# Optimization experiments

Measured on AMD Instinct MI355X. Metric: run time of the kernel, lower is better.

## Reference

```python
import jax, jax.numpy as jnp
import numpy as np

N_NODES = 100000
N_EDGES = 3200000
D_NODE = 16
D_EDGE = 8
D_HIDDEN = 16


def setup_inputs() -> dict:
    key = jax.random.key(0)
    ks = jax.random.split(key, 8)
    node_features = jax.random.normal(ks[0], (N_NODES, D_NODE), dtype=jnp.float32)
    edge_attr_e3nn = jax.random.normal(ks[1], (N_EDGES, D_EDGE), dtype=jnp.float32)
    node_attr_scalar_raw = jax.random.normal(ks[2], (N_NODES, 1), dtype=jnp.float32)
    W_msg_tp = jax.random.normal(ks[3], (D_NODE, D_EDGE, D_HIDDEN), dtype=jnp.float32)
    W_msg_lin = jax.random.normal(ks[4], (D_HIDDEN, D_HIDDEN), dtype=jnp.float32)
    W_upd_tp = jax.random.normal(ks[5], (D_NODE, D_HIDDEN, D_HIDDEN), dtype=jnp.float32)
    W_upd_lin = jax.random.normal(ks[6], (D_HIDDEN, D_NODE), dtype=jnp.float32)
    edge_index = jax.random.randint(ks[7], (2, N_EDGES), 0, N_NODES, dtype=jnp.int64)
    return {
        "node_features": node_features,
        "edge_attr_e3nn": edge_attr_e3nn,
        "node_attr_scalar_raw": node_attr_scalar_raw,
        "W_msg_tp": W_msg_tp,
        "W_msg_lin": W_msg_lin,
        "W_upd_tp": W_upd_tp,
        "W_upd_lin": W_upd_lin,
        "edge_index": edge_index,
    }


def reference(node_features, edge_attr_e3nn, node_attr_scalar_raw,
              W_msg_tp, W_msg_lin, W_upd_tp, W_upd_lin, edge_index):
    n_nodes = node_features.shape[0]
    row = edge_index[0]  # destination (aggregation target)
    col = edge_index[1]  # source (gathered neighbor)

    # fan-in normalizations (e3nn FullyConnectedTensorProduct / Linear convention)
    norm_msg_tp = 1.0 / np.float32(np.sqrt(D_NODE * D_EDGE))
    norm_upd_tp = 1.0 / np.float32(np.sqrt(D_NODE * D_HIDDEN))
    norm_lin = 1.0 / np.float32(np.sqrt(D_HIDDEN))

    # --- message step: gather -> bilinear TP -> gate -> linear ---
    x_j = node_features[col]                                   # [E, D_node]
    m = jnp.einsum('ei,ej,ijh->eh', x_j, edge_attr_e3nn, W_msg_tp) * norm_msg_tp
    m = jax.nn.silu(m)                                         # gate nonlinearity
    m = (m @ W_msg_lin) * norm_lin                             # [E, D_hidden]

    # --- scatter-sum aggregation into nodes ---
    agg = jax.ops.segment_sum(m, row, num_segments=n_nodes)    # [N, D_hidden]

    # --- update step: bilinear TP -> gate -> linear -> residual ---
    u = jnp.einsum('ni,nh,ihk->nk', node_features, agg, W_upd_tp) * norm_upd_tp
    u = jax.nn.silu(u)
    u = (u @ W_upd_lin) * norm_lin                             # [N, D_node]

    return node_features + u
```

## Files before the change

### kernel.cpp

```cpp
#include <hip/hip_runtime.h>
#include <math.h>

#define N_NODES_C 100000
#define N_EDGES_C 3200000

#define NORM_MSG_TP 0.08838834764831845f
#define NORM_UPD_TP 0.0625f
#define NORM_LIN    0.25f

typedef float f32x4 __attribute__((ext_vector_type(4)));
typedef short bf16x8 __attribute__((ext_vector_type(8)));

__device__ __forceinline__ float silu_f(float v) {
  return v / (1.0f + __expf(-v));
}

__device__ __forceinline__ void atomic_add_hw(float* p, float v) {
  unsafeAtomicAdd(p, v);
}

__device__ __forceinline__ unsigned int bf16_bits(float f) {
  unsigned int b = __float_as_uint(f);
  return (b + 0x7fffu + ((b >> 16) & 1u)) >> 16;
}
__device__ __forceinline__ unsigned int pack_bf16x2(float lo, float hi) {
  return bf16_bits(lo) | (bf16_bits(hi) << 16);
}
__device__ __forceinline__ float unlo(unsigned int w) { return __uint_as_float(w << 16); }
__device__ __forceinline__ float unhi(unsigned int w) { return __uint_as_float(w & 0xffff0000u); }


__global__ __launch_bounds__(256) void zero_ints(int* __restrict__ p, int n) {
  int i = blockIdx.x * 256 + threadIdx.x;
  if (i < n) p[i] = 0;
}

__global__ __launch_bounds__(256) void hist_kernel(
    const int* __restrict__ row, int* __restrict__ cnt) {
  int e = blockIdx.x * 256 + threadIdx.x;
  atomicAdd(&cnt[row[e]], 1);
}

__global__ __launch_bounds__(256) void scan_block(
    const int* __restrict__ cnt, int* __restrict__ off, int* __restrict__ bsum, int n) {
  __shared__ int s[256];
  const int t = threadIdx.x;
  const int i = blockIdx.x * 256 + t;
  const int v = (i < n) ? cnt[i] : 0;
  s[t] = v;
  __syncthreads();
#pragma unroll
  for (int o = 1; o < 256; o <<= 1) {
    int tv = (t >= o) ? s[t - o] : 0;
    __syncthreads();
    s[t] += tv;
    __syncthreads();
  }
  if (i < n) off[i] = s[t] - v;
  if (t == 255) bsum[blockIdx.x] = s[255];
}

__global__ void scan_bsum(int* __restrict__ bsum, int nb) {
  __shared__ int s[512];
  const int t = threadIdx.x;
  const int v = (t < nb) ? bsum[t] : 0;
  s[t] = v;
  __syncthreads();
#pragma unroll
  for (int o = 1; o < 512; o <<= 1) {
    int tv = (t >= o) ? s[t - o] : 0;
    __syncthreads();
    s[t] += tv;
    __syncthreads();
  }
  if (t < nb) bsum[t] = s[t] - v;
}

__global__ __launch_bounds__(256) void scan_add(
    int* __restrict__ off, const int* __restrict__ bsum, int n, int total) {
  int i = blockIdx.x * 256 + threadIdx.x;
  if (i < n) off[i] += bsum[blockIdx.x];
  if (i == 0) off[n] = total;
}


__global__ __launch_bounds__(256) void xcast_kernel(
    const float* __restrict__ x, unsigned short* __restrict__ xb) {
  const int i = blockIdx.x * 256 + threadIdx.x;
  if (i < N_NODES_C * 2) {
    const float4 a = *reinterpret_cast<const float4*>(x + (size_t)i * 8);
    const float4 b = *reinterpret_cast<const float4*>(x + (size_t)i * 8 + 4);
    uint4 w;
    w.x = pack_bf16x2(a.x, a.y); w.y = pack_bf16x2(a.z, a.w);
    w.z = pack_bf16x2(b.x, b.y); w.w = pack_bf16x2(b.z, b.w);
    *reinterpret_cast<uint4*>(xb + (size_t)i * 8) = w;
  }
}


__global__ __launch_bounds__(256) void place3_kernel(
    const int*   __restrict__ eidx,
    const float* __restrict__ ea,
    const float* __restrict__ Wtp,
    const int*   __restrict__ off,
    int*         __restrict__ cnt,
    const unsigned short* __restrict__ xb,
    unsigned int* __restrict__ msort)
{
  __shared__ float sm[4][16][16];
  const int lane = threadIdx.x & 63;
  const int wv   = threadIdx.x >> 6;
  const int r    = lane & 15;
  const int g    = lane >> 4;

  bf16x8 bq[4];
#pragma unroll
  for (int q = 0; q < 4; ++q) {
#pragma unroll
    for (int t = 0; t < 8; ++t) {
      const float w = Wtp[(32 * q + g * 8 + t) * 16 + r];
      bq[q][t] = (short)bf16_bits(w);
    }
  }

  const int nwaves = gridDim.x * 4;
  const int wid = blockIdx.x * 4 + wv;
  const int ntiles = N_EDGES_C / 16;

  for (int tile = wid; tile < ntiles; tile += nwaves) {
    const int e = tile * 16 + r;

    int pp = 0;
    if (g == 0) {
      const int rd = eidx[e];
      pp = off[rd] + atomicSub(&cnt[rd], 1) - 1;
    }

    const int c = eidx[N_EDGES_C + e];
    const float4 ja = *reinterpret_cast<const float4*>(ea + (size_t)e * 8);
    const float4 jb = *reinterpret_cast<const float4*>(ea + (size_t)e * 8 + 4);

    f32x4 acc = {0.f, 0.f, 0.f, 0.f};
#pragma unroll
    for (int q = 0; q < 4; ++q) {
      const float xs = __uint_as_float(
          (unsigned int)xb[(size_t)c * 16 + 4 * q + g] << 16);
      bf16x8 af;
      af[0] = (short)bf16_bits(xs * ja.x);
      af[1] = (short)bf16_bits(xs * ja.y);
      af[2] = (short)bf16_bits(xs * ja.z);
      af[3] = (short)bf16_bits(xs * ja.w);
      af[4] = (short)bf16_bits(xs * jb.x);
      af[5] = (short)bf16_bits(xs * jb.y);
      af[6] = (short)bf16_bits(xs * jb.z);
      af[7] = (short)bf16_bits(xs * jb.w);
      acc = __builtin_amdgcn_mfma_f32_16x16x32_bf16(af, bq[q], acc, 0, 0, 0);
    }

#pragma unroll
    for (int j2 = 0; j2 < 4; ++j2)
      sm[wv][g * 4 + j2][r] = silu_f(acc[j2] * NORM_MSG_TP);

    asm volatile("s_waitcnt lgkmcnt(0)" ::: "memory");
    __builtin_amdgcn_sched_barrier(0);

    const int rr  = lane >> 2;
    const int wsl = lane & 3;
    const float4 v4 = *reinterpret_cast<const float4*>(&sm[wv][rr][wsl * 4]);
    const int p_rr = __shfl(pp, rr);
    uint2 wout;
    wout.x = pack_bf16x2(v4.x, v4.y);
    wout.y = pack_bf16x2(v4.z, v4.w);
    *reinterpret_cast<uint2*>(&msort[(size_t)p_rr * 8 + wsl * 2]) = wout;
  }
}


__global__ __launch_bounds__(256) void agg3_kernel(
    const float* __restrict__ Wlin,
    const unsigned int* __restrict__ msort,
    const int*   __restrict__ off,
    float*       __restrict__ agg)
{
  __shared__ float sL[256];
  if (threadIdx.x < 256) sL[threadIdx.x] = Wlin[threadIdx.x];
  __syncthreads();

  const int slane = threadIdx.x & 15;
  const int n = blockIdx.x * 16 + (threadIdx.x >> 4);

  const int off0 = off[n];
  const int off1 = off[n + 1];

  float acc = 0.f;
  for (int p = off0; p < off1; ++p) {
    const unsigned int w = msort[(size_t)p * 8 + (slane >> 1)];
    acc += (slane & 1) ? unhi(w) : unlo(w);
  }

  float a = 0.f;
#pragma unroll
  for (int h = 0; h < 16; ++h) {
    const float v = __shfl(acc, h, 16);
    a = fmaf(v, sL[h * 16 + slane], a);
  }
  agg[(size_t)n * 16 + slane] = a * NORM_LIN;
}


__global__ __launch_bounds__(256) void tbuild_kernel(
    const float* __restrict__ x, const float* __restrict__ Wtp,
    uint4* __restrict__ Tb)
{
  __shared__ float sWT[16 * 132];
  for (int idx = threadIdx.x; idx < 2048; idx += 256) {
    const int i = idx >> 7, j = (idx >> 4) & 7, h = idx & 15;
    sWT[h * 132 + i * 8 + j] = Wtp[idx];
  }
  __syncthreads();

  const int slane = threadIdx.x & 15;
  const int n = blockIdx.x * 16 + (threadIdx.x >> 4);

  float xr[16];
  const float4* xp = reinterpret_cast<const float4*>(x + (size_t)n * 16);
#pragma unroll
  for (int q = 0; q < 4; ++q) {
    float4 v = xp[q];
    xr[q*4+0] = v.x; xr[q*4+1] = v.y; xr[q*4+2] = v.z; xr[q*4+3] = v.w;
  }

  float t[8];
#pragma unroll
  for (int j = 0; j < 8; ++j) t[j] = 0.f;
#pragma unroll
  for (int i = 0; i < 16; ++i) {
    const float xi = xr[i];
    const float4 wa = *reinterpret_cast<const float4*>(&sWT[slane * 132 + i * 8]);
    const float4 wb = *reinterpret_cast<const float4*>(&sWT[slane * 132 + i * 8 + 4]);
    t[0] = fmaf(xi, wa.x, t[0]); t[1] = fmaf(xi, wa.y, t[1]);
    t[2] = fmaf(xi, wa.z, t[2]); t[3] = fmaf(xi, wa.w, t[3]);
    t[4] = fmaf(xi, wb.x, t[4]); t[5] = fmaf(xi, wb.y, t[5]);
    t[6] = fmaf(xi, wb.z, t[6]); t[7] = fmaf(xi, wb.w, t[7]);
  }
  uint4 w;
  w.x = pack_bf16x2(t[0], t[1]);
  w.y = pack_bf16x2(t[2], t[3]);
  w.z = pack_bf16x2(t[4], t[5]);
  w.w = pack_bf16x2(t[6], t[7]);
  Tb[(size_t)n * 16 + slane] = w;
}

__global__ __launch_bounds__(256) void place_kernel(
    const int* __restrict__ eidx, const float* __restrict__ ea,
    const int* __restrict__ off, int* __restrict__ cnt,
    int* __restrict__ colp, uint4* __restrict__ eab) {
  int e = blockIdx.x * 256 + threadIdx.x;
  const int r = eidx[e];
  const int old = atomicSub(&cnt[r], 1);
  const int p = off[r] + old - 1;
  colp[p] = eidx[N_EDGES_C + e];
  const float4* ep = reinterpret_cast<const float4*>(ea + (size_t)e * 8);
  const float4 a = ep[0];
  const float4 b = ep[1];
  uint4 w;
  w.x = pack_bf16x2(a.x, a.y);
  w.y = pack_bf16x2(a.z, a.w);
  w.z = pack_bf16x2(b.x, b.y);
  w.w = pack_bf16x2(b.z, b.w);
  eab[p] = w;
}

__global__ __launch_bounds__(256) void agg2_kernel(
    const float* __restrict__ Wlin, const int* __restrict__ colp,
    const uint4* __restrict__ eab, const uint4* __restrict__ Tb,
    const int* __restrict__ off, float* __restrict__ agg)
{
  __shared__ float sL[256];
  if (threadIdx.x < 256) sL[threadIdx.x] = Wlin[threadIdx.x];
  __syncthreads();

  const int slane = threadIdx.x & 15;
  const int n = blockIdx.x * 16 + (threadIdx.x >> 4);

  const int off0 = off[n];
  const int off1 = off[n + 1];

  float acc = 0.f;
#pragma unroll 2
  for (int p = off0; p < off1; ++p) {
    const int c = colp[p];
    const uint4 tw = Tb[(size_t)c * 16 + slane];
    const uint4 ew = eab[p];
    float m;
    m  = unlo(ew.x) * unlo(tw.x);
    m  = fmaf(unhi(ew.x), unhi(tw.x), m);
    m  = fmaf(unlo(ew.y), unlo(tw.y), m);
    m  = fmaf(unhi(ew.y), unhi(tw.y), m);
    m  = fmaf(unlo(ew.z), unlo(tw.z), m);
    m  = fmaf(unhi(ew.z), unhi(tw.z), m);
    m  = fmaf(unlo(ew.w), unlo(tw.w), m);
    m  = fmaf(unhi(ew.w), unhi(tw.w), m);
    acc += silu_f(m * NORM_MSG_TP);
  }

  float a = 0.f;
#pragma unroll
  for (int h = 0; h < 16; ++h) {
    const float v = __shfl(acc, h, 16);
    a = fmaf(v, sL[h * 16 + slane], a);
  }
  agg[(size_t)n * 16 + slane] = a * NORM_LIN;
}


__global__ __launch_bounds__(256) void node_kernel(
    const float* __restrict__ x, const float* __restrict__ agg,
    const float* __restrict__ Wtp, const float* __restrict__ Wlin,
    float* __restrict__ out)
{
  __shared__ float sW[4096];
  __shared__ float sL[256];
  for (int t = threadIdx.x; t < 4096; t += 256) sW[t] = Wtp[t];
  sL[threadIdx.x] = Wlin[threadIdx.x];
  __syncthreads();

  const long n = (long)blockIdx.x * 256 + threadIdx.x;
  if (n >= N_NODES_C) return;

  float xr[16], ar[16];
  const float4* xp = reinterpret_cast<const float4*>(x + (size_t)n * 16);
  const float4* ap = reinterpret_cast<const float4*>(agg + (size_t)n * 16);
#pragma unroll
  for (int q = 0; q < 4; ++q) {
    float4 v = xp[q];
    xr[q*4+0] = v.x; xr[q*4+1] = v.y; xr[q*4+2] = v.z; xr[q*4+3] = v.w;
    float4 w = ap[q];
    ar[q*4+0] = w.x; ar[q*4+1] = w.y; ar[q*4+2] = w.z; ar[q*4+3] = w.w;
  }
  float u[16];
#pragma unroll
  for (int k = 0; k < 16; ++k) u[k] = 0.f;
#pragma unroll
  for (int i = 0; i < 16; ++i) {
#pragma unroll
    for (int h = 0; h < 16; ++h) {
      const float p = xr[i] * ar[h];
      const float* w = &sW[(i*16 + h) * 16];
#pragma unroll
      for (int k = 0; k < 16; ++k) u[k] = fmaf(p, w[k], u[k]);
    }
  }
  float g[16];
#pragma unroll
  for (int k = 0; k < 16; ++k) g[k] = silu_f(u[k] * NORM_UPD_TP);
  float res[16];
#pragma unroll
  for (int k2 = 0; k2 < 16; ++k2) {
    float a = 0.f;
#pragma unroll
    for (int k = 0; k < 16; ++k) a = fmaf(g[k], sL[k*16 + k2], a);
    res[k2] = xr[k2] + a * NORM_LIN;
  }
  float4* op = reinterpret_cast<float4*>(out + (size_t)n * 16);
#pragma unroll
  for (int q = 0; q < 4; ++q)
    op[q] = make_float4(res[q*4+0], res[q*4+1], res[q*4+2], res[q*4+3]);
}


__global__ void zero_f4(float4* __restrict__ p, int n4) {
  int i = blockIdx.x * blockDim.x + threadIdx.x;
  if (i < n4) p[i] = make_float4(0.f, 0.f, 0.f, 0.f);
}

#define EPT 2
__global__ __launch_bounds__(256) void edge_kernel(
    const float* __restrict__ x, const float* __restrict__ ea,
    const float* __restrict__ Wtp, const float* __restrict__ Wlin,
    const int* __restrict__ eidx, float* __restrict__ agg)
{
  __shared__ float sW[2048];
  __shared__ float sL[256];
  for (int t = threadIdx.x; t < 2048; t += 256) sW[t] = Wtp[t];
  sL[threadIdx.x] = Wlin[threadIdx.x];
  __syncthreads();
  const long e0 = ((long)blockIdx.x * 256 + threadIdx.x) * EPT;
  float xr[EPT][16], er[EPT][8];
  int rw[EPT];
#pragma unroll
  for (int e = 0; e < EPT; ++e) {
    const long ei = e0 + e;
    const int c = eidx[N_EDGES_C + ei];
    rw[e] = eidx[ei];
    const float4* xp = reinterpret_cast<const float4*>(x + (size_t)c * 16);
#pragma unroll
    for (int q = 0; q < 4; ++q) {
      float4 v = xp[q];
      xr[e][q*4+0] = v.x; xr[e][q*4+1] = v.y; xr[e][q*4+2] = v.z; xr[e][q*4+3] = v.w;
    }
    const float4* ep = reinterpret_cast<const float4*>(ea + (size_t)ei * 8);
#pragma unroll
    for (int q = 0; q < 2; ++q) {
      float4 v = ep[q];
      er[e][q*4+0] = v.x; er[e][q*4+1] = v.y; er[e][q*4+2] = v.z; er[e][q*4+3] = v.w;
    }
  }
  float m[EPT][16];
#pragma unroll
  for (int e = 0; e < EPT; ++e)
#pragma unroll
    for (int h = 0; h < 16; ++h) m[e][h] = 0.f;
#pragma unroll
  for (int i = 0; i < 16; ++i) {
#pragma unroll
    for (int j = 0; j < 8; ++j) {
      float p[EPT];
#pragma unroll
      for (int e = 0; e < EPT; ++e) p[e] = xr[e][i] * er[e][j];
      const float* w = &sW[(i*8 + j) * 16];
#pragma unroll
      for (int h = 0; h < 16; ++h) {
        const float wv = w[h];
#pragma unroll
        for (int e = 0; e < EPT; ++e) m[e][h] = fmaf(p[e], wv, m[e][h]);
      }
    }
  }
#pragma unroll
  for (int e = 0; e < EPT; ++e) {
    float g[16];
#pragma unroll
    for (int h = 0; h < 16; ++h) g[h] = silu_f(m[e][h] * NORM_MSG_TP);
    float* ap = agg + (size_t)rw[e] * 16;
#pragma unroll
    for (int h2 = 0; h2 < 16; ++h2) {
      float a = 0.f;
#pragma unroll
      for (int h = 0; h < 16; ++h) a = fmaf(g[h], sL[h*16 + h2], a);
      atomic_add_hw(ap + h2, a * NORM_LIN);
    }
  }
}


extern "C" void kernel_launch(void* const* d_in, const int* in_sizes, int n_in,
                              void* d_out, int out_size, void* d_ws, size_t ws_size,
                              hipStream_t stream) {
  const float* node_features = (const float*)d_in[0];
  const float* edge_attr     = (const float*)d_in[1];
  const float* W_msg_tp      = (const float*)d_in[3];
  const float* W_msg_lin     = (const float*)d_in[4];
  const float* W_upd_tp      = (const float*)d_in[5];
  const float* W_upd_lin     = (const float*)d_in[6];
  const int*   edge_index    = (const int*)d_in[7];
  float* out = (float*)d_out;
  char* ws = (char*)d_ws;

  const int NB_N = (N_NODES_C + 255) / 256;
  const int NB_E = N_EDGES_C / 256;
  const int NB_G = N_NODES_C / 16;

  const size_t A_OFF  = 0;
  const size_t A_CNT  = 400128;
  const size_t A_BSUM = 800256;
  const size_t A_MSORT= 802304;
  const size_t A_XB   = A_MSORT + 102400000;
  const size_t A_AGG  = A_XB + 3200000;
  const size_t A_NEED = A_AGG + 6400000;

  const size_t B_OFF  = 0;
  const size_t B_CNT  = 400128;
  const size_t B_BSUM = 800256;
  const size_t B_COLP = 804352;
  const size_t B_EAB  = B_COLP + 12800000;
  const size_t B_T    = B_EAB + 51200000;
  const size_t B_AGG  = B_T + 25600000;
  const size_t B_NEED = B_AGG + 6400000;

  if (ws_size >= A_NEED) {
    int*   off   = (int*)(ws + A_OFF);
    int*   cnt   = (int*)(ws + A_CNT);
    int*   bsum  = (int*)(ws + A_BSUM);
    unsigned int* msort = (unsigned int*)(ws + A_MSORT);
    unsigned short* xb  = (unsigned short*)(ws + A_XB);
    float* agg   = (float*)(ws + A_AGG);

    hipLaunchKernelGGL(zero_ints, dim3(NB_N), dim3(256), 0, stream, cnt, N_NODES_C);
    hipLaunchKernelGGL(hist_kernel, dim3(NB_E), dim3(256), 0, stream, edge_index, cnt);
    hipLaunchKernelGGL(scan_block, dim3(NB_N), dim3(256), 0, stream,
                       cnt, off, bsum, N_NODES_C);
    hipLaunchKernelGGL(scan_bsum, dim3(1), dim3(512), 0, stream, bsum, NB_N);
    hipLaunchKernelGGL(scan_add, dim3(NB_N), dim3(256), 0, stream,
                       off, bsum, N_NODES_C, N_EDGES_C);
    hipLaunchKernelGGL(xcast_kernel, dim3((N_NODES_C * 2 + 255) / 256), dim3(256),
                       0, stream, node_features, xb);
    hipLaunchKernelGGL(place3_kernel, dim3(2048), dim3(256), 0, stream,
                       edge_index, edge_attr, W_msg_tp, off, cnt, xb, msort);
    hipLaunchKernelGGL(agg3_kernel, dim3(NB_G), dim3(256), 0, stream,
                       W_msg_lin, msort, off, agg);
    hipLaunchKernelGGL(node_kernel, dim3(NB_N), dim3(256), 0, stream,
                       node_features, agg, W_upd_tp, W_upd_lin, out);
  } else if (ws_size >= B_NEED) {
    int*   off  = (int*)(ws + B_OFF);
    int*   cnt  = (int*)(ws + B_CNT);
    int*   bsum = (int*)(ws + B_BSUM);
    int*   colp = (int*)(ws + B_COLP);
    uint4* eab  = (uint4*)(ws + B_EAB);
    uint4* Tb   = (uint4*)(ws + B_T);
    float* agg  = (float*)(ws + B_AGG);

    hipLaunchKernelGGL(zero_ints, dim3(NB_N), dim3(256), 0, stream, cnt, N_NODES_C);
    hipLaunchKernelGGL(hist_kernel, dim3(NB_E), dim3(256), 0, stream, edge_index, cnt);
    hipLaunchKernelGGL(scan_block, dim3(NB_N), dim3(256), 0, stream,
                       cnt, off, bsum, N_NODES_C);
    hipLaunchKernelGGL(scan_bsum, dim3(1), dim3(512), 0, stream, bsum, NB_N);
    hipLaunchKernelGGL(scan_add, dim3(NB_N), dim3(256), 0, stream,
                       off, bsum, N_NODES_C, N_EDGES_C);
    hipLaunchKernelGGL(place_kernel, dim3(NB_E), dim3(256), 0, stream,
                       edge_index, edge_attr, off, cnt, colp, eab);
    hipLaunchKernelGGL(tbuild_kernel, dim3(NB_G), dim3(256), 0, stream,
                       node_features, W_msg_tp, Tb);
    hipLaunchKernelGGL(agg2_kernel, dim3(NB_G), dim3(256), 0, stream,
                       W_msg_lin, colp, eab, Tb, off, agg);
    hipLaunchKernelGGL(node_kernel, dim3(NB_N), dim3(256), 0, stream,
                       node_features, agg, W_upd_tp, W_upd_lin, out);
  } else {
    float* agg = (float*)ws;
    const int n4 = N_NODES_C * 16 / 4;
    hipLaunchKernelGGL(zero_f4, dim3((n4 + 255) / 256), dim3(256), 0, stream,
                       (float4*)agg, n4);
    hipLaunchKernelGGL(edge_kernel, dim3(N_EDGES_C / (256 * EPT)), dim3(256), 0, stream,
                       node_features, edge_attr, W_msg_tp, W_msg_lin, edge_index, agg);
    hipLaunchKernelGGL(node_kernel, dim3(NB_N), dim3(256), 0, stream,
                       node_features, agg, W_upd_tp, W_upd_lin, out);
  }
}
```

Baseline: 400.4 us.

## Software-pipeline edge tiles in place kernel with prefetched claims and vector gathers

Replaces place3 with place4, which claims slots and loads column indices two tiles ahead and gathers node features and edge attributes one tile ahead, so the atomic and gather latencies overlap with MFMA work. Each gather becomes a 16-byte vector load by half the lanes, redistributed with shuffles, and the MFMA K ordering and weight layout are permuted to match. bf16 packing now uses round-half-up plus a byte permute instead of round-to-nearest-even, and the shared tile is padded against bank conflicts. The cost is more registers and shuffles, plus slightly different rounding.

```diff
diff --git a/kernel.cpp b/kernel.cpp
--- a/kernel.cpp
+++ b/kernel.cpp
@@ -10,6 +10,7 @@
 
 typedef float f32x4 __attribute__((ext_vector_type(4)));
 typedef short bf16x8 __attribute__((ext_vector_type(8)));
+typedef int   int4v  __attribute__((ext_vector_type(4)));
 
 __device__ __forceinline__ float silu_f(float v) {
   return v / (1.0f + __expf(-v));
@@ -98,7 +99,25 @@
 }
 
 
-__global__ __launch_bounds__(256) void place3_kernel(
+#define CLAIM_TILE(T, CC, PP) do {                                   \
+    const int e_ = (T) * 16 + r;                                     \
+    if (g == 0) {                                                    \
+      CC = eidx[N_EDGES_C + e_];                                     \
+      const int rd_ = eidx[e_];                                      \
+      PP = off[rd_] + atomicSub(&cnt[rd_], 1) - 1;                   \
+    }                                                                \
+  } while (0)
+
+#define GATH_TILE(T, CC, XH, F4) do {                                \
+    const int e_ = (T) * 16 + r;                                     \
+    const int c_ = __shfl(CC, r);                                    \
+    if (g < 2) {                                                     \
+      XH = *reinterpret_cast<const uint4*>(xb + (size_t)c_ * 16 + g * 8); \
+      F4 = *reinterpret_cast<const float4*>(ea + (size_t)e_ * 8 + g * 4); \
+    }                                                                \
+  } while (0)
+
+__global__ __launch_bounds__(256) void place4_kernel(
     const int*   __restrict__ eidx,
     const float* __restrict__ ea,
     const float* __restrict__ Wtp,
@@ -107,54 +126,80 @@
     const unsigned short* __restrict__ xb,
     unsigned int* __restrict__ msort)
 {
-  __shared__ float sm[4][16][16];
-  const int lane = threadIdx.x & 63;
-  const int wv   = threadIdx.x >> 6;
-  const int r    = lane & 15;
-  const int g    = lane >> 4;
+  __shared__ float sm[4][16][20];
+  const int lane  = threadIdx.x & 63;
+  const int wv    = threadIdx.x >> 6;
+  const int r     = lane & 15;
+  const int g     = lane >> 4;
+  const int gsel  = g >> 1;
+  const int ghalf = g & 1;
 
   bf16x8 bq[4];
 #pragma unroll
   for (int q = 0; q < 4; ++q) {
 #pragma unroll
     for (int t = 0; t < 8; ++t) {
-      const float w = Wtp[(32 * q + g * 8 + t) * 16 + r];
+      const float w = Wtp[(8 * ghalf + t) * 128 + (2 * q + gsel) * 16 + r];
       bq[q][t] = (short)bf16_bits(w);
     }
   }
 
-  const int nwaves = gridDim.x * 4;
+  const int s = gridDim.x * 4;
   const int wid = blockIdx.x * 4 + wv;
   const int ntiles = N_EDGES_C / 16;
 
-  for (int tile = wid; tile < ntiles; tile += nwaves) {
-    const int e = tile * 16 + r;
-
-    int pp = 0;
-    if (g == 0) {
-      const int rd = eidx[e];
-      pp = off[rd] + atomicSub(&cnt[rd], 1) - 1;
-    }
-
-    const int c = eidx[N_EDGES_C + e];
-    const float4 ja = *reinterpret_cast<const float4*>(ea + (size_t)e * 8);
-    const float4 jb = *reinterpret_cast<const float4*>(ea + (size_t)e * 8 + 4);
+  int cc_a = 0, pp_a = 0, cc_b = 0, pp_b = 0;
+  uint4 xh_a; xh_a.x = xh_a.y = xh_a.z = xh_a.w = 0;
+  float4 f4_a = make_float4(0.f, 0.f, 0.f, 0.f);
+
+  if (wid < ntiles)     CLAIM_TILE(wid, cc_a, pp_a);
+  if (wid + s < ntiles) CLAIM_TILE(wid + s, cc_b, pp_b);
+  if (wid < ntiles)     GATH_TILE(wid, cc_a, xh_a, f4_a);
+
+  for (int t = wid; t < ntiles; t += s) {
+    int cc_c = 0, pp_c = 0;
+    if (t + 2 * s < ntiles) CLAIM_TILE(t + 2 * s, cc_c, pp_c);
+    uint4 xh_b; xh_b.x = xh_b.y = xh_b.z = xh_b.w = 0;
+    float4 f4_b = make_float4(0.f, 0.f, 0.f, 0.f);
+    if (t + s < ntiles) GATH_TILE(t + s, cc_b, xh_b, f4_b);
+
+    uint4 xh;
+    xh.x = (unsigned)__shfl((int)xh_a.x, ghalf * 16 + r);
+    xh.y = (unsigned)__shfl((int)xh_a.y, ghalf * 16 + r);
+    xh.z = (unsigned)__shfl((int)xh_a.z, ghalf * 16 + r);
+    xh.w = (unsigned)__shfl((int)xh_a.w, ghalf * 16 + r);
+    float xf[8];
+    xf[0] = unlo(xh.x); xf[1] = unhi(xh.x);
+    xf[2] = unlo(xh.y); xf[3] = unhi(xh.y);
+    xf[4] = unlo(xh.z); xf[5] = unhi(xh.z);
+    xf[6] = unlo(xh.w); xf[7] = unhi(xh.w);
+    const float a0 = __shfl(f4_a.x, r),      a1 = __shfl(f4_a.y, r);
+    const float a2 = __shfl(f4_a.z, r),      a3 = __shfl(f4_a.w, r);
+    const float b0 = __shfl(f4_a.x, 16 + r), b1 = __shfl(f4_a.y, 16 + r);
+    const float b2 = __shfl(f4_a.z, 16 + r), b3 = __shfl(f4_a.w, 16 + r);
+    float eq[4];
+    eq[0] = gsel ? a1 : a0;  eq[1] = gsel ? a3 : a2;
+    eq[2] = gsel ? b1 : b0;  eq[3] = gsel ? b3 : b2;
 
     f32x4 acc = {0.f, 0.f, 0.f, 0.f};
 #pragma unroll
     for (int q = 0; q < 4; ++q) {
-      const float xs = __uint_as_float(
-          (unsigned int)xb[(size_t)c * 16 + 4 * q + g] << 16);
-      bf16x8 af;
-      af[0] = (short)bf16_bits(xs * ja.x);
-      af[1] = (short)bf16_bits(xs * ja.y);
-      af[2] = (short)bf16_bits(xs * ja.z);
-      af[3] = (short)bf16_bits(xs * ja.w);
-      af[4] = (short)bf16_bits(xs * jb.x);
-      af[5] = (short)bf16_bits(xs * jb.y);
-      af[6] = (short)bf16_bits(xs * jb.z);
-      af[7] = (short)bf16_bits(xs * jb.w);
-      acc = __builtin_amdgcn_mfma_f32_16x16x32_bf16(af, bq[q], acc, 0, 0, 0);
+      const float e_ = eq[q];
+      const unsigned u0 = __float_as_uint(xf[0] * e_) + 0x8000u;
+      const unsigned u1 = __float_as_uint(xf[1] * e_) + 0x8000u;
+      const unsigned u2 = __float_as_uint(xf[2] * e_) + 0x8000u;
+      const unsigned u3 = __float_as_uint(xf[3] * e_) + 0x8000u;
+      const unsigned u4 = __float_as_uint(xf[4] * e_) + 0x8000u;
+      const unsigned u5 = __float_as_uint(xf[5] * e_) + 0x8000u;
+      const unsigned u6 = __float_as_uint(xf[6] * e_) + 0x8000u;
+      const unsigned u7 = __float_as_uint(xf[7] * e_) + 0x8000u;
+      int4v iv;
+      iv.x = (int)__builtin_amdgcn_perm(u1, u0, 0x07060302u);
+      iv.y = (int)__builtin_amdgcn_perm(u3, u2, 0x07060302u);
+      iv.z = (int)__builtin_amdgcn_perm(u5, u4, 0x07060302u);
+      iv.w = (int)__builtin_amdgcn_perm(u7, u6, 0x07060302u);
+      union { int4v i; bf16x8 h; } cv; cv.i = iv;
+      acc = __builtin_amdgcn_mfma_f32_16x16x32_bf16(cv.h, bq[q], acc, 0, 0, 0);
     }
 
 #pragma unroll
@@ -167,11 +212,14 @@
     const int rr  = lane >> 2;
     const int wsl = lane & 3;
     const float4 v4 = *reinterpret_cast<const float4*>(&sm[wv][rr][wsl * 4]);
-    const int p_rr = __shfl(pp, rr);
+    const int prr = __shfl(pp_a, rr);
     uint2 wout;
     wout.x = pack_bf16x2(v4.x, v4.y);
     wout.y = pack_bf16x2(v4.z, v4.w);
-    *reinterpret_cast<uint2*>(&msort[(size_t)p_rr * 8 + wsl * 2]) = wout;
+    *reinterpret_cast<uint2*>(&msort[(size_t)prr * 8 + wsl * 2]) = wout;
+
+    pp_a = pp_b; xh_a = xh_b; f4_a = f4_b;
+    cc_b = cc_c; pp_b = pp_c;
   }
 }
 
@@ -495,7 +543,7 @@
                        off, bsum, N_NODES_C, N_EDGES_C);
     hipLaunchKernelGGL(xcast_kernel, dim3((N_NODES_C * 2 + 255) / 256), dim3(256),
                        0, stream, node_features, xb);
-    hipLaunchKernelGGL(place3_kernel, dim3(2048), dim3(256), 0, stream,
+    hipLaunchKernelGGL(place4_kernel, dim3(2048), dim3(256), 0, stream,
                        edge_index, edge_attr, W_msg_tp, off, cnt, xb, msort);
     hipLaunchKernelGGL(agg3_kernel, dim3(NB_G), dim3(256), 0, stream,
                        W_msg_lin, msort, off, agg);
```

New measurement: 381.7 us. 1.05x faster.
